# Kernel tuning notes

Measured on AMD Instinct MI355X. Metric: run time of the kernel, lower is better.

The kernel has to match this reference:

```python
import jax, jax.numpy as jnp
import numpy as np

A0 = 0.529177249
SIGMA = jnp.array([0.5515909, 1.8886297, 1.3225029, 1.2316629,
                   2.1884933, 1.7750372, 1.3677907, 1.3820058], dtype=jnp.float32)


def celu(x):
    return jax.nn.celu(x, alpha=0.1)


def setup_inputs() -> dict:
    key = jax.random.key(0)
    ks = jax.random.split(key, 24)
    N, n, L, E = 512, 64, 384, 8
    H1, H2, H3 = 160, 128, 96
    s = 0.05
    f32 = jnp.float32
    return {
        "species": jax.random.randint(ks[0], (N, n), 0, E, dtype=jnp.int32),
        "coordinates": 3.0 * jax.random.normal(ks[1], (N, n, 3), dtype=f32),
        "net_charge": jax.random.normal(ks[2], (N,), dtype=f32),
        "aev": jax.random.normal(ks[3], (N, n, L), dtype=f32),
        "chi_W1": s * jax.random.normal(ks[4], (L, H1), dtype=f32),
        "chi_b1": s * jax.random.normal(ks[5], (H1,), dtype=f32),
        "chi_W2": s * jax.random.normal(ks[6], (H1, H2), dtype=f32),
        "chi_b2": s * jax.random.normal(ks[7], (H2,), dtype=f32),
        "chi_W3": s * jax.random.normal(ks[8], (H2, H3), dtype=f32),
        "chi_b3": s * jax.random.normal(ks[9], (H3,), dtype=f32),
        "chi_W4": s * jax.random.normal(ks[10], (H3, 1), dtype=f32),
        "chi_b4": s * jax.random.normal(ks[11], (1,), dtype=f32),
        "W1": s * jax.random.normal(ks[12], (E, L + 2, H1), dtype=f32),
        "b1": s * jax.random.normal(ks[13], (E, H1), dtype=f32),
        "W2": s * jax.random.normal(ks[14], (E, H1, H2), dtype=f32),
        "b2": s * jax.random.normal(ks[15], (E, H2), dtype=f32),
        "W3": s * jax.random.normal(ks[16], (E, H2, H3), dtype=f32),
        "b3": s * jax.random.normal(ks[17], (E, H3), dtype=f32),
        "W4": s * jax.random.normal(ks[18], (E, H3), dtype=f32),
        "b4": s * jax.random.normal(ks[19], (E,), dtype=f32),
    }


def _forward(species, coordinates, net_charge, aev,
             chi_W1, chi_b1, chi_W2, chi_b2, chi_W3, chi_b3, chi_W4, chi_b4,
             W1, b1, W2, b2, W3, b3, W4, b4):
    N, n = species.shape
    aev_flat = aev.reshape(N * n, -1)                       # (A, L)

    # nonzero_batch_dmat: distances in atomic units, eps avoids div-by-zero
    diff = coordinates[:, None, :, :] - coordinates[:, :, None, :]
    dist = jnp.sqrt(jnp.sum(diff * diff, -1) + 1e-16) / A0   # (N, n, n)

    pad = (species != -1).astype(aev.dtype)                  # (N, n)
    pair_mask = pad[:, None, :] * pad[:, :, None]            # (N, n, n)
    num_atoms = pad.sum(axis=1)                              # (N,)
    valid = (species.reshape(-1) != -1)                      # (A,)

    # chi_net: 4-layer MLP (CELU 0.1) + Softplus, masked to valid atoms
    h = celu(aev_flat @ chi_W1 + chi_b1)
    h = celu(h @ chi_W2 + chi_b2)
    h = celu(h @ chi_W3 + chi_b3)
    chi = jax.nn.softplus(h @ chi_W4 + chi_b4)[:, 0]
    chi = jnp.where(valid, chi, 0.0).reshape(N, n)

    chi_sum = chi.sum(axis=-1)
    k_net = 1.0 + jnp.abs(net_charge) / chi_sum
    chi_mean = chi_sum / num_atoms
    k_p = jnp.where(net_charge > 0, k_net, 1.0)
    k_n = jnp.where(net_charge < 0, k_net, 1.0)
    q = (-k_n[:, None] * chi + (k_p * chi_mean)[:, None]) * pad  # (N, n)

    # ESPerf: pairwise erf-screened Coulomb potential
    sig = SIGMA[jnp.clip(species, 0)]                        # (N, n)
    sig_sqsum = sig[:, None, :] ** 2 + sig[:, :, None] ** 2
    sig_sqsum = jnp.maximum(sig_sqsum, 1e-8)
    j_ij = jax.scipy.special.erf(dist / jnp.sqrt(2.0 * sig_sqsum)) / dist
    diag_mask = 1.0 - jnp.eye(n, dtype=dist.dtype)
    esp = (q[:, :, None] * j_ij * pair_mask * diag_mask[None]).sum(axis=-2)  # (N, n)
    coulomb_energy = 0.5 * (q * esp).sum(axis=-1)            # (N,)

    # species-routed expert MLPs over [aev | charge | esp] features
    feat = jnp.concatenate(
        [aev_flat, q.reshape(-1, 1), esp.reshape(-1, 1)], axis=1)  # (A, L+2)
    h1 = celu(jnp.einsum('ad,edh->aeh', feat, W1) + b1)      # (A, E, H1)
    h2 = celu(jnp.einsum('aeh,ehk->aek', h1, W2) + b2)       # (A, E, H2)
    h3 = celu(jnp.einsum('aek,ekm->aem', h2, W3) + b3)       # (A, E, H3)
    out_all = jnp.einsum('aem,em->ae', h3, W4) + b4          # (A, E)

    sp = jnp.clip(species.reshape(-1), 0)
    out = jnp.take_along_axis(out_all, sp[:, None], axis=1)[:, 0]
    out = jnp.where(valid, out, 0.0).reshape(N, n)
    mol_energy = out.sum(axis=1)
    return species, mol_energy + coulomb_energy, q


def reference(species, coordinates, net_charge, aev,
              chi_W1, chi_b1, chi_W2, chi_b2, chi_W3, chi_b3, chi_W4, chi_b4,
              W1, b1, W2, b2, W3, b3, W4, b4):
    return _forward(species, coordinates, net_charge, aev,
                    chi_W1, chi_b1, chi_W2, chi_b2, chi_W3, chi_b3, chi_W4, chi_b4,
                    W1, b1, W2, b2, W3, b3, W4, b4)
```

## Files before the change

kernel.cpp:

```cpp
#include <hip/hip_runtime.h>
#include <math.h>

#define A0_INV (1.0f/0.529177249f)

typedef __bf16 bf16x8 __attribute__((ext_vector_type(8)));
typedef __bf16 bf16x4 __attribute__((ext_vector_type(4)));
typedef float  f32x4  __attribute__((ext_vector_type(4)));

__device__ __constant__ float c_SIGMA[8] = {
    0.5515909f, 1.8886297f, 1.3225029f, 1.2316629f,
    2.1884933f, 1.7750372f, 1.3677907f, 1.3820058f};

__device__ __forceinline__ float celu01(float x) {
    return x > 0.0f ? x : 0.1f * (__expf(x * 10.0f) - 1.0f);
}
__device__ __forceinline__ float softplusf_(float x) {
    return fmaxf(x, 0.0f) + log1pf(__expf(-fabsf(x)));
}
__device__ __forceinline__ __bf16 u16_to_bf16(unsigned short u) {
    __bf16 b; __builtin_memcpy(&b, &u, 2); return b;
}
__device__ __forceinline__ unsigned short f_to_bf16_bits(float f) {
    __bf16 b = (__bf16)f; unsigned short u; __builtin_memcpy(&u, &b, 2); return u;
}

__device__ __forceinline__ void pack_one(int idx, const float* __restrict__ W,
                                         __bf16* __restrict__ Bp,
                                         int K, int OUT, int NT, int KT)
{
    int lane = idx & 63;
    int rest = idx >> 6;
    int kt = rest % KT; rest /= KT;
    int nt = rest % NT;
    int e  = rest / NT;
    int col = nt * 16 + (lane & 15);
    int k0  = kt * 32 + (lane >> 4) * 8;
    bf16x8 o;
#pragma unroll
    for (int j = 0; j < 8; ++j) {
        int k = k0 + j;
        float v = (k < K) ? W[((long)e * K + k) * OUT + col] : 0.0f;
        o[j] = (__bf16)v;
    }
    *((bf16x8*)Bp + idx) = o;
}

__global__ __launch_bounds__(256) void pack_all_kernel(
    const float* __restrict__ cW1, const float* __restrict__ cW2, const float* __restrict__ cW3,
    const float* __restrict__ W1,  const float* __restrict__ W2,  const float* __restrict__ W3,
    __bf16* bp_c1, __bf16* bp_c2, __bf16* bp_c3,
    __bf16* bp_e1, __bf16* bp_e2, __bf16* bp_e3)
{
    int idx = blockIdx.x * 256 + threadIdx.x;
    if      (idx <   7680) pack_one(idx,          cW1, bp_c1, 384, 160, 10, 12);
    else if (idx <  10240) pack_one(idx - 7680,   cW2, bp_c2, 160, 128,  8,  5);
    else if (idx <  11776) pack_one(idx - 10240,  cW3, bp_c3, 128,  96,  6,  4);
    else if (idx <  78336) pack_one(idx - 11776,  W1,  bp_e1, 386, 160, 10, 13);
    else if (idx <  98816) pack_one(idx - 78336,  W2,  bp_e2, 160, 128,  8,  5);
    else if (idx < 111104) pack_one(idx - 98816,  W3,  bp_e3, 128,  96,  6,  4);
}

template<int NT, int KT, int INS, int OUTS, bool CELU>
__device__ __forceinline__ void mlp_layer8(const __bf16* sIn, const bf16x8* __restrict__ Bp,
                                           const float* __restrict__ bias, __bf16* sOut, int tid)
{
    const int lane = tid & 63;
    const int wid  = tid >> 6;
    const int mw   = wid >> 2;
    const int nw   = wid & 3;
    const int r16  = lane & 15;
    const int g    = lane >> 4;
    constexpr int NJ = (NT + 3) / 4;
    f32x4 acc[2][NJ];
#pragma unroll
    for (int mi = 0; mi < 2; ++mi)
#pragma unroll
        for (int j = 0; j < NJ; ++j)
            acc[mi][j] = (f32x4){0.f, 0.f, 0.f, 0.f};

    bf16x8 bcur[NJ], bnxt[NJ];
#pragma unroll
    for (int j = 0; j < NJ; ++j) {
        const int nt = nw + 4 * j;
        if (nt < NT) bcur[j] = Bp[(nt * KT) * 64 + lane];
    }
    for (int kt = 0; kt < KT; ++kt) {
        bf16x8 a[2];
#pragma unroll
        for (int mi = 0; mi < 2; ++mi)
            a[mi] = *(const bf16x8*)(sIn + ((mw * 2 + mi) * 16 + r16) * INS + kt * 32 + g * 8);
        if (kt + 1 < KT) {
#pragma unroll
            for (int j = 0; j < NJ; ++j) {
                const int nt = nw + 4 * j;
                if (nt < NT) bnxt[j] = Bp[(nt * KT + kt + 1) * 64 + lane];
            }
        }
#pragma unroll
        for (int j = 0; j < NJ; ++j) {
            const int nt = nw + 4 * j;
            if (nt < NT) {
#pragma unroll
                for (int mi = 0; mi < 2; ++mi)
                    acc[mi][j] = __builtin_amdgcn_mfma_f32_16x16x32_bf16(a[mi], bcur[j], acc[mi][j], 0, 0, 0);
            }
        }
#pragma unroll
        for (int j = 0; j < NJ; ++j) bcur[j] = bnxt[j];
    }
#pragma unroll
    for (int j = 0; j < NJ; ++j) {
        const int nt = nw + 4 * j;
        if (nt < NT) {
            const float bb = bias[nt * 16 + r16];
#pragma unroll
            for (int mi = 0; mi < 2; ++mi)
#pragma unroll
                for (int r = 0; r < 4; ++r) {
                    float v = acc[mi][j][r] + bb;
                    if (CELU) v = celu01(v);
                    sOut[((mw * 2 + mi) * 16 + g * 4 + r) * OUTS + nt * 16 + r16] = (__bf16)v;
                }
        }
    }
}

__device__ __forceinline__ float l4_dot(const __bf16* __restrict__ h,
                                        const float* __restrict__ w4)
{
    float acc = 0.f;
#pragma unroll
    for (int u8 = 0; u8 < 12; ++u8) {
        bf16x8 hv = *(const bf16x8*)(h + u8 * 8);
        float4 wa = *(const float4*)(w4 + u8 * 8);
        float4 wb = *(const float4*)(w4 + u8 * 8 + 4);
        acc = fmaf((float)hv[0], wa.x, acc);
        acc = fmaf((float)hv[1], wa.y, acc);
        acc = fmaf((float)hv[2], wa.z, acc);
        acc = fmaf((float)hv[3], wa.w, acc);
        acc = fmaf((float)hv[4], wb.x, acc);
        acc = fmaf((float)hv[5], wb.y, acc);
        acc = fmaf((float)hv[6], wb.z, acc);
        acc = fmaf((float)hv[7], wb.w, acc);
    }
    return acc;
}

__global__ __launch_bounds__(512) void chimol_kernel(
    const float* __restrict__ aev, const int* __restrict__ species,
    const float* __restrict__ coords, const float* __restrict__ netq,
    const __bf16* __restrict__ bp1, const __bf16* __restrict__ bp2, const __bf16* __restrict__ bp3,
    const float* __restrict__ b1, const float* __restrict__ b2, const float* __restrict__ b3,
    const float* __restrict__ W4, const float* __restrict__ b4,
    __bf16* __restrict__ aev16,
    int* __restrict__ blockCounts, int* __restrict__ rank,
    float* __restrict__ qv, float* __restrict__ esp, float* __restrict__ coul,
    float* __restrict__ o_species, float* __restrict__ o_q)
{
    __shared__ __align__(16) unsigned char smem[50176 + 21504];
    __shared__ float sChi[64];
    __shared__ float sx[64], sy[64], sz[64], sq[64], ss2[64];
    __shared__ float sEsp[8][64];
    __bf16* sFeat = (__bf16*)smem;
    __bf16* sAct1 = (__bf16*)(smem + 50176);
    __bf16* sAct2 = (__bf16*)smem;
    __bf16* sAct3 = (__bf16*)(smem + 17408);
    const int t = threadIdx.x;
    const int m = blockIdx.x;
    const long base = (long)m * 64;

    if (aev16) {
        for (int i = t; i < 64 * 96; i += 512) {
            int row = i / 96, c4 = (i - row * 96) * 4;
            float4 v = *(const float4*)(aev + (base + row) * 384 + c4);
            bf16x4 o = {(__bf16)v.x, (__bf16)v.y, (__bf16)v.z, (__bf16)v.w};
            *(bf16x4*)(sFeat + row * 392 + c4) = o;
            *(bf16x4*)(aev16 + (base + row) * 384 + c4) = o;
        }
    } else {
        for (int i = t; i < 64 * 96; i += 512) {
            int row = i / 96, c4 = (i - row * 96) * 4;
            float4 v = *(const float4*)(aev + (base + row) * 384 + c4);
            bf16x4 o = {(__bf16)v.x, (__bf16)v.y, (__bf16)v.z, (__bf16)v.w};
            *(bf16x4*)(sFeat + row * 392 + c4) = o;
        }
    }
    __syncthreads();
    mlp_layer8<10, 12, 392, 168, true>(sFeat, (const bf16x8*)bp1, b1, sAct1, t);
    __syncthreads();
    mlp_layer8<8, 5, 168, 136, true>(sAct1, (const bf16x8*)bp2, b2, sAct2, t);
    __syncthreads();
    mlp_layer8<6, 4, 136, 104, true>(sAct2, (const bf16x8*)bp3, b3, sAct3, t);
    __syncthreads();
    if (t < 64) {
        float acc = l4_dot(sAct3 + t * 104, W4);
        float chiv = softplusf_(acc + b4[0]);
        long atom = base + t;
        int s = species[atom];
        if (s == -1) chiv = 0.f;
        sChi[t] = chiv;
        unsigned long long mym = 0;
#pragma unroll
        for (int e = 0; e < 8; ++e) {
            unsigned long long bm = __ballot(s == e);
            if (t == e) blockCounts[m * 8 + e] = (int)__popcll(bm);
            if (s == e) mym = bm;
        }
        if (s >= 0) rank[atom] = (int)__popcll(mym & ((1ull << t) - 1ull));
    }
    __syncthreads();

    const int j = t & 63, grp = t >> 6;
    const int atom = (int)base + j;
    int s = species[atom];
    float pad = (s != -1) ? 1.0f : 0.0f;
    float chij = sChi[j];

    float cs = chij, na = pad;
#pragma unroll
    for (int o = 32; o > 0; o >>= 1) {
        cs += __shfl_xor(cs, o);
        na += __shfl_xor(na, o);
    }
    float qc = netq[m];
    float k_net = 1.0f + fabsf(qc) / cs;
    float chi_mean = cs / na;
    float k_p = (qc > 0.0f) ? k_net : 1.0f;
    float k_n = (qc < 0.0f) ? k_net : 1.0f;
    float qj = (-k_n * chij + k_p * chi_mean) * pad;

    float sg = c_SIGMA[s < 0 ? 0 : s];
    float x = coords[atom * 3 + 0], y = coords[atom * 3 + 1], z = coords[atom * 3 + 2];
    if (grp == 0) { sx[j] = x; sy[j] = y; sz[j] = z; sq[j] = qj; ss2[j] = sg * sg; }
    __syncthreads();

    float s2j = sg * sg;
    float ej = 0.0f;
#pragma unroll
    for (int k = 0; k < 8; ++k) {
        int i = grp * 8 + k;
        if (i == j) continue;
        float dx = sx[i] - x, dy = sy[i] - y, dz = sz[i] - z;
        float d = sqrtf(dx * dx + dy * dy + dz * dz + 1e-16f) * A0_INV;
        float ssum = fmaxf(ss2[i] + s2j, 1e-8f);
        float jij = erff(d * rsqrtf(2.0f * ssum)) / d;
        ej = fmaf(sq[i], jij, ej);
    }
    sEsp[grp][j] = ej;
    __syncthreads();
    if (grp == 0) {
        float e = ((sEsp[0][j] + sEsp[1][j]) + (sEsp[2][j] + sEsp[3][j]))
                + ((sEsp[4][j] + sEsp[5][j]) + (sEsp[6][j] + sEsp[7][j]));
        e *= pad;
        float ce = qj * e;
#pragma unroll
        for (int o = 32; o > 0; o >>= 1) ce += __shfl_xor(ce, o);
        if (j == 0) coul[m] = 0.5f * ce;
        qv[atom] = qj;
        esp[atom] = e;
        o_species[atom] = (float)s;
        o_q[atom] = qj;
    }
}

__global__ void bucket_scan_kernel(int* __restrict__ blockCounts,
                                   int* __restrict__ counts, int* __restrict__ offs,
                                   int* __restrict__ workItems, int* __restrict__ workCount,
                                   int nb)
{
    __shared__ int segSum[8][8];
    __shared__ int tot[8];
    const int tid = threadIdx.x;
    const int seg = tid >> 3, e = tid & 7;
    const int per = (nb + 7) / 8;
    const int b0 = seg * per, b1 = min(b0 + per, nb);
    int run = 0;
    for (int b = b0; b < b1; ++b) run += blockCounts[b * 8 + e];
    segSum[seg][e] = run;
    __syncthreads();
    if (tid < 8) {
        int r = 0;
        for (int s2 = 0; s2 < 8; ++s2) { int c = segSum[s2][tid]; segSum[s2][tid] = r; r += c; }
        tot[tid] = r;
    }
    __syncthreads();
    int runp = segSum[seg][e];
    for (int b = b0; b < b1; ++b) {
        int c = blockCounts[b * 8 + e];
        blockCounts[b * 8 + e] = runp;
        runp += c;
    }
    if (tid == 0) {
        int o = 0;
        for (int i = 0; i < 8; ++i) { offs[i] = o; counts[i] = tot[i]; o += tot[i]; }
        offs[8] = o;
    }
    if (tid < 8) {
        int pos = 0;
        for (int i = 0; i < tid; ++i) pos += (tot[i] + 63) >> 6;
        int nt_e = (tot[tid] + 63) >> 6;
        for (int k = 0; k < nt_e; ++k) workItems[pos + k] = (tid << 20) | (k * 64);
        if (tid == 7) workCount[0] = pos + nt_e;
    }
}

__global__ __launch_bounds__(256) void bucket_fill_kernel(
    const int* __restrict__ species, const int* __restrict__ blockCounts,
    const int* __restrict__ offs, const int* __restrict__ rank,
    int* __restrict__ bidx, float* __restrict__ outat, int A)
{
    int a = blockIdx.x * 256 + threadIdx.x;
    if (a < A) {
        outat[a] = 0.0f;
        int s = species[a];
        if (s >= 0)
            bidx[offs[s] + blockCounts[(a >> 6) * 8 + s] + rank[a]] = a;
    }
}

__device__ __forceinline__ bf16x8 loadA16(const __bf16* __restrict__ aev16,
                                          int atom, int kt, int g)
{
    bf16x8 z = {};
    if (atom < 0) return z;
    return *(const bf16x8*)(aev16 + (long)atom * 384 + kt * 32 + g * 8);
}
__device__ __forceinline__ bf16x8 loadAf(const float* __restrict__ aev,
                                         int atom, int kt, int g)
{
    bf16x8 z = {};
    if (atom < 0) return z;
    const float* p = aev + (long)atom * 384 + kt * 32 + g * 8;
    float4 va = *(const float4*)p, vb = *(const float4*)(p + 4);
    bf16x8 r = {(__bf16)va.x, (__bf16)va.y, (__bf16)va.z, (__bf16)va.w,
                (__bf16)vb.x, (__bf16)vb.y, (__bf16)vb.z, (__bf16)vb.w};
    return r;
}

template<bool HAVE16>
__global__ __launch_bounds__(512, 4) void expert_mfma_kernel(
    const float* __restrict__ aev, const __bf16* __restrict__ aev16,
    const float* __restrict__ qv, const float* __restrict__ esp,
    const __bf16* __restrict__ bp1, const __bf16* __restrict__ bp2, const __bf16* __restrict__ bp3,
    const float* __restrict__ b1, const float* __restrict__ b2, const float* __restrict__ b3,
    const float* __restrict__ W4, const float* __restrict__ b4,
    const int* __restrict__ counts, const int* __restrict__ offs, const int* __restrict__ bidx,
    const int* __restrict__ workItems, const int* __restrict__ workCount,
    float* __restrict__ outat)
{
    const int bid = blockIdx.x;
    if (bid >= workCount[0]) return;
    const int wi = workItems[bid];
    const int e = wi >> 20;
    const int start = wi & 0xFFFFF;
    const int cnt = counts[e];

    __shared__ __align__(16) unsigned char smem[21504 + 17408];
    __shared__ int said[64];
    __shared__ unsigned int sQE[64];
    __bf16* sAct1 = (__bf16*)smem;
    __bf16* sAct2 = (__bf16*)(smem + 21504);
    __bf16* sAct3 = (__bf16*)smem;
    const int t = threadIdx.x;

    if (t < 64) {
        int a_ = (start + t < cnt) ? bidx[offs[e] + start + t] : -1;
        said[t] = a_;
        float q = 0.f, es = 0.f;
        if (a_ >= 0) { q = qv[a_]; es = esp[a_]; }
        sQE[t] = ((unsigned)f_to_bf16_bits(es) << 16) | f_to_bf16_bits(q);
    }
    __syncthreads();

    {
        const int lane = t & 63, wid = t >> 6;
        const int mw = wid >> 2, nw = wid & 3;
        const int r16 = lane & 15, g = lane >> 4;
        const int atom0 = said[(mw * 2 + 0) * 16 + r16];
        const int atom1 = said[(mw * 2 + 1) * 16 + r16];
        const bf16x8* Bp = (const bf16x8*)bp1 + (size_t)e * 10 * 13 * 64;
        constexpr int NJ = 3;
        f32x4 acc[2][NJ];
#pragma unroll
        for (int mi = 0; mi < 2; ++mi)
#pragma unroll
            for (int j = 0; j < NJ; ++j) acc[mi][j] = (f32x4){0.f, 0.f, 0.f, 0.f};

        bf16x8 bcur[NJ], bnxt[NJ];
#pragma unroll
        for (int j = 0; j < NJ; ++j) {
            const int nt = nw + 4 * j;
            if (nt < 10) bcur[j] = Bp[(nt * 13) * 64 + lane];
        }
        bf16x8 a0c = HAVE16 ? loadA16(aev16, atom0, 0, g) : loadAf(aev, atom0, 0, g);
        bf16x8 a1c = HAVE16 ? loadA16(aev16, atom1, 0, g) : loadAf(aev, atom1, 0, g);

        for (int kt = 0; kt < 12; ++kt) {
#pragma unroll
            for (int j = 0; j < NJ; ++j) {
                const int nt = nw + 4 * j;
                if (nt < 10) bnxt[j] = Bp[(nt * 13 + kt + 1) * 64 + lane];
            }
            bf16x8 a0n, a1n;
            if (kt < 11) {
                a0n = HAVE16 ? loadA16(aev16, atom0, kt + 1, g) : loadAf(aev, atom0, kt + 1, g);
                a1n = HAVE16 ? loadA16(aev16, atom1, kt + 1, g) : loadAf(aev, atom1, kt + 1, g);
            }
#pragma unroll
            for (int j = 0; j < NJ; ++j) {
                const int nt = nw + 4 * j;
                if (nt < 10) {
                    acc[0][j] = __builtin_amdgcn_mfma_f32_16x16x32_bf16(a0c, bcur[j], acc[0][j], 0, 0, 0);
                    acc[1][j] = __builtin_amdgcn_mfma_f32_16x16x32_bf16(a1c, bcur[j], acc[1][j], 0, 0, 0);
                }
            }
#pragma unroll
            for (int j = 0; j < NJ; ++j) bcur[j] = bnxt[j];
            if (kt < 11) { a0c = a0n; a1c = a1n; }
        }
        bf16x8 aq0 = {}, aq1 = {};
        if (g == 0) {
            unsigned qe0 = sQE[(mw * 2 + 0) * 16 + r16];
            unsigned qe1 = sQE[(mw * 2 + 1) * 16 + r16];
            aq0[0] = u16_to_bf16((unsigned short)(qe0 & 0xffff));
            aq0[1] = u16_to_bf16((unsigned short)(qe0 >> 16));
            aq1[0] = u16_to_bf16((unsigned short)(qe1 & 0xffff));
            aq1[1] = u16_to_bf16((unsigned short)(qe1 >> 16));
        }
#pragma unroll
        for (int j = 0; j < NJ; ++j) {
            const int nt = nw + 4 * j;
            if (nt < 10) {
                acc[0][j] = __builtin_amdgcn_mfma_f32_16x16x32_bf16(aq0, bcur[j], acc[0][j], 0, 0, 0);
                acc[1][j] = __builtin_amdgcn_mfma_f32_16x16x32_bf16(aq1, bcur[j], acc[1][j], 0, 0, 0);
            }
        }
#pragma unroll
        for (int j = 0; j < NJ; ++j) {
            const int nt = nw + 4 * j;
            if (nt < 10) {
                const float bb = b1[e * 160 + nt * 16 + r16];
#pragma unroll
                for (int mi = 0; mi < 2; ++mi)
#pragma unroll
                    for (int r = 0; r < 4; ++r) {
                        float v = acc[mi][j][r] + bb;
                        v = celu01(v);
                        sAct1[((mw * 2 + mi) * 16 + g * 4 + r) * 168 + nt * 16 + r16] = (__bf16)v;
                    }
            }
        }
    }
    __syncthreads();
    mlp_layer8<8, 5, 168, 136, true>(sAct1, (const bf16x8*)bp2 + (size_t)e * 8 * 5 * 64,
                                     b2 + e * 128, sAct2, t);
    __syncthreads();
    mlp_layer8<6, 4, 136, 104, true>(sAct2, (const bf16x8*)bp3 + (size_t)e * 6 * 4 * 64,
                                     b3 + e * 96, sAct3, t);
    __syncthreads();
    if (t < 64) {
        int atom = said[t];
        if (atom >= 0) {
            float acc = l4_dot(sAct3 + t * 104, W4 + e * 96);
            outat[atom] = acc + b4[e];
        }
    }
}

__global__ __launch_bounds__(64) void energy_kernel(
    const float* __restrict__ outat, const float* __restrict__ coul,
    float* __restrict__ o_energy)
{
    int m = blockIdx.x, t = threadIdx.x;
    float v = outat[m * 64 + t];
#pragma unroll
    for (int o = 32; o > 0; o >>= 1) v += __shfl_xor(v, o);
    if (t == 0) o_energy[m] = v + coul[m];
}

extern "C" void kernel_launch(void* const* d_in, const int* in_sizes, int n_in,
                              void* d_out, int out_size, void* d_ws, size_t ws_size,
                              hipStream_t stream)
{
    const int*   species = (const int*)  d_in[0];
    const float* coords  = (const float*)d_in[1];
    const float* netq    = (const float*)d_in[2];
    const float* aev     = (const float*)d_in[3];
    const float* cW1 = (const float*)d_in[4];
    const float* cb1 = (const float*)d_in[5];
    const float* cW2 = (const float*)d_in[6];
    const float* cb2 = (const float*)d_in[7];
    const float* cW3 = (const float*)d_in[8];
    const float* cb3 = (const float*)d_in[9];
    const float* cW4 = (const float*)d_in[10];
    const float* cb4 = (const float*)d_in[11];
    const float* W1  = (const float*)d_in[12];
    const float* b1  = (const float*)d_in[13];
    const float* W2  = (const float*)d_in[14];
    const float* b2  = (const float*)d_in[15];
    const float* W3  = (const float*)d_in[16];
    const float* b3  = (const float*)d_in[17];
    const float* W4  = (const float*)d_in[18];
    const float* b4  = (const float*)d_in[19];

    const int N = in_sizes[2];
    const int n = in_sizes[0] / N;
    const int A = N * n;
    const int nb64 = A / 64;
    const int maxWork = nb64 + 8;

    float* fbase   = (float*)d_ws;
    float* qv      = fbase;
    float* esp     = fbase + (size_t)A;
    float* outat   = fbase + (size_t)2 * A;
    float* coul    = fbase + (size_t)3 * A;
    int*   counts  = (int*)(coul + N);
    int*   offs    = counts + 8;
    int*   workCount = offs + 9;
    int*   workItems = workCount + 1;
    int*   blockCounts = workItems + maxWork;
    int*   rank    = blockCounts + nb64 * 8;
    int*   bidx    = rank + A;
    uintptr_t p = ((uintptr_t)(bidx + A) + 15) & ~(uintptr_t)15;
    __bf16* bp_c1 = (__bf16*)p; p += (size_t)10 * 12 * 512 * 2;
    __bf16* bp_c2 = (__bf16*)p; p += (size_t)8  * 5  * 512 * 2;
    __bf16* bp_c3 = (__bf16*)p; p += (size_t)6  * 4  * 512 * 2;
    __bf16* bp_e1 = (__bf16*)p; p += (size_t)8 * 10 * 13 * 512 * 2;
    __bf16* bp_e2 = (__bf16*)p; p += (size_t)8 * 8  * 5  * 512 * 2;
    __bf16* bp_e3 = (__bf16*)p; p += (size_t)8 * 6  * 4  * 512 * 2;
    p = (p + 15) & ~(uintptr_t)15;
    __bf16* aev16 = (__bf16*)p;
    size_t need = (p - (uintptr_t)d_ws) + (size_t)A * 384 * 2;
    if (ws_size < need) aev16 = nullptr;

    float* o_species = (float*)d_out;
    float* o_energy  = o_species + A;
    float* o_q       = o_energy + N;

    pack_all_kernel<<<(111104 + 255) / 256, 256, 0, stream>>>(
        cW1, cW2, cW3, W1, W2, W3, bp_c1, bp_c2, bp_c3, bp_e1, bp_e2, bp_e3);

    chimol_kernel<<<nb64, 512, 0, stream>>>(aev, species, coords, netq,
                                            bp_c1, bp_c2, bp_c3,
                                            cb1, cb2, cb3, cW4, cb4,
                                            aev16, blockCounts, rank,
                                            qv, esp, coul, o_species, o_q);
    bucket_scan_kernel<<<1, 64, 0, stream>>>(blockCounts, counts, offs,
                                             workItems, workCount, nb64);
    bucket_fill_kernel<<<(A + 255) / 256, 256, 0, stream>>>(species, blockCounts, offs,
                                                            rank, bidx, outat, A);
    if (aev16)
        expert_mfma_kernel<true><<<maxWork, 512, 0, stream>>>(
            aev, aev16, qv, esp, bp_e1, bp_e2, bp_e3, b1, b2, b3, W4, b4,
            counts, offs, bidx, workItems, workCount, outat);
    else
        expert_mfma_kernel<false><<<maxWork, 512, 0, stream>>>(
            aev, aev16, qv, esp, bp_e1, bp_e2, bp_e3, b1, b2, b3, W4, b4,
            counts, offs, bidx, workItems, workCount, outat);
    energy_kernel<<<N, 64, 0, stream>>>(outat, coul, o_energy);
}
```

Baseline: 94.94 us.

## Double block size to 1024 threads with one 16-row tile per wave

Raises the block size of the chi-network and expert kernels from 512 to 1024 threads, giving each wave a single 16-row M tile instead of two, and splits the ESP pair loop into 16 groups instead of 8. The software prefetch of B fragments and A rows across k steps is removed, so each MFMA now loads its weights directly from global memory. The aim is more waves per block to hide latency, at the cost of losing explicit prefetch, reloading B fragments per wave with half the reuse, and a larger block with higher register pressure under the 1024-thread bound.

```diff
diff --git a/kernel.cpp b/kernel.cpp
--- a/kernel.cpp
+++ b/kernel.cpp
@@ -61,8 +61,8 @@
 }
 
 template<int NT, int KT, int INS, int OUTS, bool CELU>
-__device__ __forceinline__ void mlp_layer8(const __bf16* sIn, const bf16x8* __restrict__ Bp,
-                                           const float* __restrict__ bias, __bf16* sOut, int tid)
+__device__ __forceinline__ void mlp_layer16(const __bf16* sIn, const bf16x8* __restrict__ Bp,
+                                            const float* __restrict__ bias, __bf16* sOut, int tid)
 {
     const int lane = tid & 63;
     const int wid  = tid >> 6;
@@ -71,42 +71,20 @@
     const int r16  = lane & 15;
     const int g    = lane >> 4;
     constexpr int NJ = (NT + 3) / 4;
-    f32x4 acc[2][NJ];
-#pragma unroll
-    for (int mi = 0; mi < 2; ++mi)
-#pragma unroll
-        for (int j = 0; j < NJ; ++j)
-            acc[mi][j] = (f32x4){0.f, 0.f, 0.f, 0.f};
-
-    bf16x8 bcur[NJ], bnxt[NJ];
-#pragma unroll
-    for (int j = 0; j < NJ; ++j) {
-        const int nt = nw + 4 * j;
-        if (nt < NT) bcur[j] = Bp[(nt * KT) * 64 + lane];
-    }
+    f32x4 acc[NJ];
+#pragma unroll
+    for (int j = 0; j < NJ; ++j) acc[j] = (f32x4){0.f, 0.f, 0.f, 0.f};
+
     for (int kt = 0; kt < KT; ++kt) {
-        bf16x8 a[2];
-#pragma unroll
-        for (int mi = 0; mi < 2; ++mi)
-            a[mi] = *(const bf16x8*)(sIn + ((mw * 2 + mi) * 16 + r16) * INS + kt * 32 + g * 8);
-        if (kt + 1 < KT) {
-#pragma unroll
-            for (int j = 0; j < NJ; ++j) {
-                const int nt = nw + 4 * j;
-                if (nt < NT) bnxt[j] = Bp[(nt * KT + kt + 1) * 64 + lane];
-            }
-        }
+        bf16x8 a = *(const bf16x8*)(sIn + (mw * 16 + r16) * INS + kt * 32 + g * 8);
 #pragma unroll
         for (int j = 0; j < NJ; ++j) {
             const int nt = nw + 4 * j;
             if (nt < NT) {
-#pragma unroll
-                for (int mi = 0; mi < 2; ++mi)
-                    acc[mi][j] = __builtin_amdgcn_mfma_f32_16x16x32_bf16(a[mi], bcur[j], acc[mi][j], 0, 0, 0);
+                bf16x8 b = Bp[(nt * KT + kt) * 64 + lane];
+                acc[j] = __builtin_amdgcn_mfma_f32_16x16x32_bf16(a, b, acc[j], 0, 0, 0);
             }
         }
-#pragma unroll
-        for (int j = 0; j < NJ; ++j) bcur[j] = bnxt[j];
     }
 #pragma unroll
     for (int j = 0; j < NJ; ++j) {
@@ -114,13 +92,11 @@
         if (nt < NT) {
             const float bb = bias[nt * 16 + r16];
 #pragma unroll
-            for (int mi = 0; mi < 2; ++mi)
-#pragma unroll
-                for (int r = 0; r < 4; ++r) {
-                    float v = acc[mi][j][r] + bb;
-                    if (CELU) v = celu01(v);
-                    sOut[((mw * 2 + mi) * 16 + g * 4 + r) * OUTS + nt * 16 + r16] = (__bf16)v;
-                }
+            for (int r = 0; r < 4; ++r) {
+                float v = acc[j][r] + bb;
+                if (CELU) v = celu01(v);
+                sOut[(mw * 16 + g * 4 + r) * OUTS + nt * 16 + r16] = (__bf16)v;
+            }
         }
     }
 }
@@ -146,7 +122,7 @@
     return acc;
 }
 
-__global__ __launch_bounds__(512) void chimol_kernel(
+__global__ __launch_bounds__(1024, 8) void chimol_kernel(
     const float* __restrict__ aev, const int* __restrict__ species,
     const float* __restrict__ coords, const float* __restrict__ netq,
     const __bf16* __restrict__ bp1, const __bf16* __restrict__ bp2, const __bf16* __restrict__ bp3,
@@ -160,7 +136,7 @@
     __shared__ __align__(16) unsigned char smem[50176 + 21504];
     __shared__ float sChi[64];
     __shared__ float sx[64], sy[64], sz[64], sq[64], ss2[64];
-    __shared__ float sEsp[8][64];
+    __shared__ float sEsp[16][64];
     __bf16* sFeat = (__bf16*)smem;
     __bf16* sAct1 = (__bf16*)(smem + 50176);
     __bf16* sAct2 = (__bf16*)smem;
@@ -170,7 +146,7 @@
     const long base = (long)m * 64;
 
     if (aev16) {
-        for (int i = t; i < 64 * 96; i += 512) {
+        for (int i = t; i < 64 * 96; i += 1024) {
             int row = i / 96, c4 = (i - row * 96) * 4;
             float4 v = *(const float4*)(aev + (base + row) * 384 + c4);
             bf16x4 o = {(__bf16)v.x, (__bf16)v.y, (__bf16)v.z, (__bf16)v.w};
@@ -178,7 +154,7 @@
             *(bf16x4*)(aev16 + (base + row) * 384 + c4) = o;
         }
     } else {
-        for (int i = t; i < 64 * 96; i += 512) {
+        for (int i = t; i < 64 * 96; i += 1024) {
             int row = i / 96, c4 = (i - row * 96) * 4;
             float4 v = *(const float4*)(aev + (base + row) * 384 + c4);
             bf16x4 o = {(__bf16)v.x, (__bf16)v.y, (__bf16)v.z, (__bf16)v.w};
@@ -186,11 +162,11 @@
         }
     }
     __syncthreads();
-    mlp_layer8<10, 12, 392, 168, true>(sFeat, (const bf16x8*)bp1, b1, sAct1, t);
-    __syncthreads();
-    mlp_layer8<8, 5, 168, 136, true>(sAct1, (const bf16x8*)bp2, b2, sAct2, t);
-    __syncthreads();
-    mlp_layer8<6, 4, 136, 104, true>(sAct2, (const bf16x8*)bp3, b3, sAct3, t);
+    mlp_layer16<10, 12, 392, 168, true>(sFeat, (const bf16x8*)bp1, b1, sAct1, t);
+    __syncthreads();
+    mlp_layer16<8, 5, 168, 136, true>(sAct1, (const bf16x8*)bp2, b2, sAct2, t);
+    __syncthreads();
+    mlp_layer16<6, 4, 136, 104, true>(sAct2, (const bf16x8*)bp3, b3, sAct3, t);
     __syncthreads();
     if (t < 64) {
         float acc = l4_dot(sAct3 + t * 104, W4);
@@ -237,8 +213,8 @@
     float s2j = sg * sg;
     float ej = 0.0f;
 #pragma unroll
-    for (int k = 0; k < 8; ++k) {
-        int i = grp * 8 + k;
+    for (int k = 0; k < 4; ++k) {
+        int i = grp * 4 + k;
         if (i == j) continue;
         float dx = sx[i] - x, dy = sy[i] - y, dz = sz[i] - z;
         float d = sqrtf(dx * dx + dy * dy + dz * dz + 1e-16f) * A0_INV;
@@ -249,8 +225,9 @@
     sEsp[grp][j] = ej;
     __syncthreads();
     if (grp == 0) {
-        float e = ((sEsp[0][j] + sEsp[1][j]) + (sEsp[2][j] + sEsp[3][j]))
-                + ((sEsp[4][j] + sEsp[5][j]) + (sEsp[6][j] + sEsp[7][j]));
+        float e = 0.f;
+#pragma unroll
+        for (int g2 = 0; g2 < 16; ++g2) e += sEsp[g2][j];
         e *= pad;
         float ce = qj * e;
 #pragma unroll
@@ -338,7 +315,7 @@
 }
 
 template<bool HAVE16>
-__global__ __launch_bounds__(512, 4) void expert_mfma_kernel(
+__global__ __launch_bounds__(1024, 8) void expert_mfma_kernel(
     const float* __restrict__ aev, const __bf16* __restrict__ aev16,
     const float* __restrict__ qv, const float* __restrict__ esp,
     const __bf16* __restrict__ bp1, const __bf16* __restrict__ bp2, const __bf16* __restrict__ bp3,
@@ -376,63 +353,36 @@
         const int lane = t & 63, wid = t >> 6;
         const int mw = wid >> 2, nw = wid & 3;
         const int r16 = lane & 15, g = lane >> 4;
-        const int atom0 = said[(mw * 2 + 0) * 16 + r16];
-        const int atom1 = said[(mw * 2 + 1) * 16 + r16];
+        const int atom0 = said[mw * 16 + r16];
         const bf16x8* Bp = (const bf16x8*)bp1 + (size_t)e * 10 * 13 * 64;
         constexpr int NJ = 3;
-        f32x4 acc[2][NJ];
-#pragma unroll
-        for (int mi = 0; mi < 2; ++mi)
-#pragma unroll
-            for (int j = 0; j < NJ; ++j) acc[mi][j] = (f32x4){0.f, 0.f, 0.f, 0.f};
-
-        bf16x8 bcur[NJ], bnxt[NJ];
-#pragma unroll
-        for (int j = 0; j < NJ; ++j) {
-            const int nt = nw + 4 * j;
-            if (nt < 10) bcur[j] = Bp[(nt * 13) * 64 + lane];
-        }
-        bf16x8 a0c = HAVE16 ? loadA16(aev16, atom0, 0, g) : loadAf(aev, atom0, 0, g);
-        bf16x8 a1c = HAVE16 ? loadA16(aev16, atom1, 0, g) : loadAf(aev, atom1, 0, g);
+        f32x4 acc[NJ];
+#pragma unroll
+        for (int j = 0; j < NJ; ++j) acc[j] = (f32x4){0.f, 0.f, 0.f, 0.f};
 
         for (int kt = 0; kt < 12; ++kt) {
-#pragma unroll
-            for (int j = 0; j < NJ; ++j) {
-                const int nt = nw + 4 * j;
-                if (nt < 10) bnxt[j] = Bp[(nt * 13 + kt + 1) * 64 + lane];
-            }
-            bf16x8 a0n, a1n;
-            if (kt < 11) {
-                a0n = HAVE16 ? loadA16(aev16, atom0, kt + 1, g) : loadAf(aev, atom0, kt + 1, g);
-                a1n = HAVE16 ? loadA16(aev16, atom1, kt + 1, g) : loadAf(aev, atom1, kt + 1, g);
-            }
+            bf16x8 a0 = HAVE16 ? loadA16(aev16, atom0, kt, g) : loadAf(aev, atom0, kt, g);
 #pragma unroll
             for (int j = 0; j < NJ; ++j) {
                 const int nt = nw + 4 * j;
                 if (nt < 10) {
-                    acc[0][j] = __builtin_amdgcn_mfma_f32_16x16x32_bf16(a0c, bcur[j], acc[0][j], 0, 0, 0);
-                    acc[1][j] = __builtin_amdgcn_mfma_f32_16x16x32_bf16(a1c, bcur[j], acc[1][j], 0, 0, 0);
+                    bf16x8 b = Bp[(nt * 13 + kt) * 64 + lane];
+                    acc[j] = __builtin_amdgcn_mfma_f32_16x16x32_bf16(a0, b, acc[j], 0, 0, 0);
                 }
             }
-#pragma unroll
-            for (int j = 0; j < NJ; ++j) bcur[j] = bnxt[j];
-            if (kt < 11) { a0c = a0n; a1c = a1n; }
-        }
-        bf16x8 aq0 = {}, aq1 = {};
+        }
+        bf16x8 aq0 = {};
         if (g == 0) {
-            unsigned qe0 = sQE[(mw * 2 + 0) * 16 + r16];
-            unsigned qe1 = sQE[(mw * 2 + 1) * 16 + r16];
+            unsigned qe0 = sQE[mw * 16 + r16];
             aq0[0] = u16_to_bf16((unsigned short)(qe0 & 0xffff));
             aq0[1] = u16_to_bf16((unsigned short)(qe0 >> 16));
-            aq1[0] = u16_to_bf16((unsigned short)(qe1 & 0xffff));
-            aq1[1] = u16_to_bf16((unsigned short)(qe1 >> 16));
         }
 #pragma unroll
         for (int j = 0; j < NJ; ++j) {
             const int nt = nw + 4 * j;
             if (nt < 10) {
-                acc[0][j] = __builtin_amdgcn_mfma_f32_16x16x32_bf16(aq0, bcur[j], acc[0][j], 0, 0, 0);
-                acc[1][j] = __builtin_amdgcn_mfma_f32_16x16x32_bf16(aq1, bcur[j], acc[1][j], 0, 0, 0);
+                bf16x8 b = Bp[(nt * 13 + 12) * 64 + lane];
+                acc[j] = __builtin_amdgcn_mfma_f32_16x16x32_bf16(aq0, b, acc[j], 0, 0, 0);
             }
         }
 #pragma unroll
@@ -441,22 +391,20 @@
             if (nt < 10) {
                 const float bb = b1[e * 160 + nt * 16 + r16];
 #pragma unroll
-                for (int mi = 0; mi < 2; ++mi)
-#pragma unroll
-                    for (int r = 0; r < 4; ++r) {
-                        float v = acc[mi][j][r] + bb;
-                        v = celu01(v);
-                        sAct1[((mw * 2 + mi) * 16 + g * 4 + r) * 168 + nt * 16 + r16] = (__bf16)v;
-                    }
+                for (int r = 0; r < 4; ++r) {
+                    float v = acc[j][r] + bb;
+                    v = celu01(v);
+                    sAct1[(mw * 16 + g * 4 + r) * 168 + nt * 16 + r16] = (__bf16)v;
+                }
             }
         }
     }
     __syncthreads();
-    mlp_layer8<8, 5, 168, 136, true>(sAct1, (const bf16x8*)bp2 + (size_t)e * 8 * 5 * 64,
-                                     b2 + e * 128, sAct2, t);
-    __syncthreads();
-    mlp_layer8<6, 4, 136, 104, true>(sAct2, (const bf16x8*)bp3 + (size_t)e * 6 * 4 * 64,
-                                     b3 + e * 96, sAct3, t);
+    mlp_layer16<8, 5, 168, 136, true>(sAct1, (const bf16x8*)bp2 + (size_t)e * 8 * 5 * 64,
+                                      b2 + e * 128, sAct2, t);
+    __syncthreads();
+    mlp_layer16<6, 4, 136, 104, true>(sAct2, (const bf16x8*)bp3 + (size_t)e * 6 * 4 * 64,
+                                      b3 + e * 96, sAct3, t);
     __syncthreads();
     if (t < 64) {
         int atom = said[t];
@@ -540,21 +488,21 @@
     pack_all_kernel<<<(111104 + 255) / 256, 256, 0, stream>>>(
         cW1, cW2, cW3, W1, W2, W3, bp_c1, bp_c2, bp_c3, bp_e1, bp_e2, bp_e3);
 
-    chimol_kernel<<<nb64, 512, 0, stream>>>(aev, species, coords, netq,
-                                            bp_c1, bp_c2, bp_c3,
-                                            cb1, cb2, cb3, cW4, cb4,
-                                            aev16, blockCounts, rank,
-                                            qv, esp, coul, o_species, o_q);
+    chimol_kernel<<<nb64, 1024, 0, stream>>>(aev, species, coords, netq,
+                                             bp_c1, bp_c2, bp_c3,
+                                             cb1, cb2, cb3, cW4, cb4,
+                                             aev16, blockCounts, rank,
+                                             qv, esp, coul, (float*)d_out, o_q);
     bucket_scan_kernel<<<1, 64, 0, stream>>>(blockCounts, counts, offs,
                                              workItems, workCount, nb64);
     bucket_fill_kernel<<<(A + 255) / 256, 256, 0, stream>>>(species, blockCounts, offs,
                                                             rank, bidx, outat, A);
     if (aev16)
-        expert_mfma_kernel<true><<<maxWork, 512, 0, stream>>>(
+        expert_mfma_kernel<true><<<maxWork, 1024, 0, stream>>>(
             aev, aev16, qv, esp, bp_e1, bp_e2, bp_e3, b1, b2, b3, W4, b4,
             counts, offs, bidx, workItems, workCount, outat);
     else
-        expert_mfma_kernel<false><<<maxWork, 512, 0, stream>>>(
+        expert_mfma_kernel<false><<<maxWork, 1024, 0, stream>>>(
             aev, aev16, qv, esp, bp_e1, bp_e2, bp_e3, b1, b2, b3, W4, b4,
             counts, offs, bidx, workItems, workCount, outat);
     energy_kernel<<<N, 64, 0, stream>>>(outat, coul, o_energy);
```

After: 108.1 us. 13.8% more time.
